# Optimization experiments

Measured on AMD Instinct MI355X. Metric: run time of the kernel, lower is better.

The kernel has to match this reference:

```python
import jax, jax.numpy as jnp
import numpy as np

N_NODES = 100000
N_EDGES = 1600000
IN_DIM, HID_DIM, OUT_DIM = 512, 128, 64


def gcn_layer(x, rows, cols, vals, W, b):
    # support = x @ W; out[i] = sum_{e: rows[e]==i} vals[e] * support[cols[e]] + b
    support = x @ W                      # [N, d_out]
    msgs = vals[:, None] * support[cols]  # [E, d_out] gather
    agg = jax.ops.segment_sum(msgs, rows, num_segments=N_NODES)  # scatter-add
    return agg + b


def setup_inputs() -> dict:
    key = jax.random.key(0)
    ks = jax.random.split(key, 8)
    x = jax.random.normal(ks[0], (N_NODES, IN_DIM), dtype=jnp.float32)
    edge_rows = jax.random.randint(ks[1], (N_EDGES,), 0, N_NODES, dtype=jnp.int32)
    edge_cols = jax.random.randint(ks[2], (N_EDGES,), 0, N_NODES, dtype=jnp.int32)
    edge_vals = jax.random.uniform(ks[3], (N_EDGES,), dtype=jnp.float32)
    W0 = jax.random.normal(ks[4], (IN_DIM, HID_DIM), dtype=jnp.float32) / np.sqrt(IN_DIM)
    b0 = jnp.zeros((HID_DIM,), dtype=jnp.float32)
    W1 = jax.random.normal(ks[5], (HID_DIM, OUT_DIM), dtype=jnp.float32) / np.sqrt(HID_DIM)
    b1 = jnp.zeros((OUT_DIM,), dtype=jnp.float32)
    return {"x": x, "edge_rows": edge_rows, "edge_cols": edge_cols,
            "edge_vals": edge_vals, "W0": W0, "b0": b0, "W1": W1, "b1": b1}


def reference(x, edge_rows, edge_cols, edge_vals, W0, b0, W1, b1):
    h = gcn_layer(x, edge_rows, edge_cols, edge_vals, W0, b0)  # GCN0
    h = jax.nn.relu(h)                                          # activation0
    # dropout: identity in eval mode
    out = gcn_layer(h, edge_rows, edge_cols, edge_vals, W1, b1)  # GCN1
    return out
```

## Files before the change

kernel.cpp:

```cpp
#include <hip/hip_runtime.h>

#define N_NODES 100000
#define N_EDGES 1600000
#define NBUCK   ((N_NODES + 127) / 128)
#define BCAP    4096

typedef __attribute__((ext_vector_type(8))) short bf16x8;
typedef __attribute__((ext_vector_type(4))) float f32x4;

__device__ __forceinline__ unsigned short f2bf(float f) {
    unsigned int u = __builtin_bit_cast(unsigned int, f);
    u = (u + 0x7FFFu + ((u >> 16) & 1u)) >> 16;
    return (unsigned short)u;
}
__device__ __forceinline__ float bfu2f(unsigned short u) {
    return __builtin_bit_cast(float, (unsigned int)u << 16);
}
__device__ __forceinline__ uint2 packbf4(float4 v) {
    uint2 p;
    p.x = (unsigned int)f2bf(v.x) | ((unsigned int)f2bf(v.y) << 16);
    p.y = (unsigned int)f2bf(v.z) | ((unsigned int)f2bf(v.w) << 16);
    return p;
}

__device__ __forceinline__ void block_barrier() {
    asm volatile("s_waitcnt lgkmcnt(0)" ::: "memory");
    __builtin_amdgcn_sched_barrier(0);
    __builtin_amdgcn_s_barrier();
    __builtin_amdgcn_sched_barrier(0);
}

__global__ __launch_bounds__(256) void prep_kernel(const float* __restrict__ W0,
                                                   const float* __restrict__ W1,
                                                   unsigned short* __restrict__ W0t,
                                                   unsigned short* __restrict__ W1t,
                                                   int* __restrict__ bcursor) {
    const int i = blockIdx.x * 256 + threadIdx.x;
    if (i < 512 * 128) {
        const int k = i / 128, c = i % 128;
        W0t[c * 512 + k] = f2bf(W0[i]);
    }
    const int j = i - 512 * 128;
    if (j >= 0 && j < 128 * 64) {
        const int k = j / 64, c = j % 64;
        W1t[c * 128 + k] = f2bf(W1[j]);
    }
    const int z = i - (512 * 128 + 128 * 64);
    if (z >= 0 && z < NBUCK) bcursor[z] = z * BCAP;
}

__global__ __launch_bounds__(256) void gemm1_kernel(const float* __restrict__ A,
                                                    const unsigned short* __restrict__ Wt,
                                                    unsigned short* __restrict__ C, int N) {
    constexpr int K   = 512;
    constexpr int M   = 128;
    constexpr int LDT = 40;

    __shared__ __align__(16) unsigned short As[2][64 * LDT];
    __shared__ __align__(16) unsigned short Bs[2][M * LDT];

    const int tid  = threadIdx.x;
    const int lane = tid & 63;
    const int wid  = tid >> 6;
    const int wm   = wid >> 1;
    const int wn   = wid & 1;
    const int brow = blockIdx.x * 64;

    const int ar0 = tid >> 3, akq = tid & 7;
    const int ar1 = ar0 + 32;
    const bool v0 = (brow + ar0) < N;
    const bool v1 = (brow + ar1) < N;
    const float* ap0 = A + (size_t)(brow + ar0) * K + akq * 4;
    const float* ap1 = A + (size_t)(brow + ar1) * K + akq * 4;
    const int br0 = tid >> 2, bkq = tid & 3;
    const unsigned short* bp0 = Wt + (size_t)br0 * K + bkq * 8;
    const unsigned short* bp1 = Wt + (size_t)(br0 + 64) * K + bkq * 8;

    float4 A0a, A0b, A1a, A1b, A2a, A2b, A3a, A3b;
    uint4  B0a, B0b, B1a, B1b, B2a, B2b, B3a, B3b;

#define ISSUE(s, t) do {                                                          \
        const int ko = (t) * 32;                                                  \
        A##s##a = v0 ? *reinterpret_cast<const float4*>(ap0 + ko)                 \
                     : make_float4(0.f, 0.f, 0.f, 0.f);                           \
        A##s##b = v1 ? *reinterpret_cast<const float4*>(ap1 + ko)                 \
                     : make_float4(0.f, 0.f, 0.f, 0.f);                           \
        B##s##a = *reinterpret_cast<const uint4*>(bp0 + ko);                      \
        B##s##b = *reinterpret_cast<const uint4*>(bp1 + ko);                      \
    } while (0)

#define WLDS(s, buf) do {                                                         \
        *reinterpret_cast<uint2*>(&As[buf][ar0 * LDT + akq * 4]) = packbf4(A##s##a); \
        *reinterpret_cast<uint2*>(&As[buf][ar1 * LDT + akq * 4]) = packbf4(A##s##b); \
        *reinterpret_cast<uint4*>(&Bs[buf][br0 * LDT + bkq * 8]) = B##s##a;          \
        *reinterpret_cast<uint4*>(&Bs[buf][(br0 + 64) * LDT + bkq * 8]) = B##s##b;   \
    } while (0)

    f32x4 acc[2][4];
#pragma unroll
    for (int m = 0; m < 2; ++m)
#pragma unroll
        for (int n = 0; n < 4; ++n) acc[m][n] = (f32x4){0.f, 0.f, 0.f, 0.f};

    const int afo = (wm * 32 + (lane & 15)) * LDT + (lane >> 4) * 8;
    const int bfo = (wn * 64 + (lane & 15)) * LDT + (lane >> 4) * 8;

    auto step = [&](int buf) {
        bf16x8 af[2], bfr[4];
#pragma unroll
        for (int m = 0; m < 2; ++m)
            af[m] = *reinterpret_cast<const bf16x8*>(&As[buf][afo + m * 16 * LDT]);
#pragma unroll
        for (int n = 0; n < 4; ++n)
            bfr[n] = *reinterpret_cast<const bf16x8*>(&Bs[buf][bfo + n * 16 * LDT]);
#pragma unroll
        for (int m = 0; m < 2; ++m)
#pragma unroll
            for (int n = 0; n < 4; ++n)
                acc[m][n] = __builtin_amdgcn_mfma_f32_16x16x32_bf16(af[m], bfr[n], acc[m][n], 0, 0, 0);
    };

    ISSUE(0, 0); ISSUE(1, 1); ISSUE(2, 2); ISSUE(3, 3);
    WLDS(0, 0);
    block_barrier();

#pragma unroll
    for (int i = 0; i < 4; ++i) {
        const int t = 4 * i;
        if (t + 4 < 16) ISSUE(0, t + 4);
        step(0);
        WLDS(1, 1);
        block_barrier();
        if (t + 5 < 16) ISSUE(1, t + 5);
        step(1);
        WLDS(2, 0);
        block_barrier();
        if (t + 6 < 16) ISSUE(2, t + 6);
        step(0);
        WLDS(3, 1);
        block_barrier();
        if (t + 7 < 16) ISSUE(3, t + 7);
        step(1);
        if (t + 4 < 16) WLDS(0, 0);
        block_barrier();
    }
#undef ISSUE
#undef WLDS

    const int rb = brow + wm * 32 + ((lane >> 4) * 4);
    const int cb = wn * 64 + (lane & 15);
#pragma unroll
    for (int m = 0; m < 2; ++m)
#pragma unroll
        for (int n = 0; n < 4; ++n)
#pragma unroll
            for (int j = 0; j < 4; ++j) {
                const int r = rb + m * 16 + j;
                if (r < N) C[(size_t)r * M + cb + n * 16] = f2bf(acc[m][n][j]);
            }
}

__global__ __launch_bounds__(256) void gemm2_kernel(const unsigned short* __restrict__ Hb,
                                                    const unsigned short* __restrict__ Wt,
                                                    unsigned short* __restrict__ C) {
    const int gw = (blockIdx.x * 256 + threadIdx.x) >> 6;
    if (gw >= N_NODES / 16) return;
    const int lane = threadIdx.x & 63;
    const int rlo = lane & 15, khi = lane >> 4;
    const int rb = gw * 16;

    const unsigned short* wp = Wt + (size_t)rlo * 128 + khi * 8;
    bf16x8 b[4][4];
#pragma unroll
    for (int n = 0; n < 4; ++n)
#pragma unroll
        for (int t = 0; t < 4; ++t)
            b[n][t] = *reinterpret_cast<const bf16x8*>(wp + (size_t)n * 16 * 128 + t * 32);

    f32x4 acc[4];
#pragma unroll
    for (int n = 0; n < 4; ++n) acc[n] = (f32x4){0.f, 0.f, 0.f, 0.f};

    const unsigned short* hp = Hb + (size_t)(rb + rlo) * 128 + khi * 8;
#pragma unroll
    for (int t = 0; t < 4; ++t) {
        const bf16x8 af = *reinterpret_cast<const bf16x8*>(hp + t * 32);
#pragma unroll
        for (int n = 0; n < 4; ++n)
            acc[n] = __builtin_amdgcn_mfma_f32_16x16x32_bf16(af, b[n][t], acc[n], 0, 0, 0);
    }

#pragma unroll
    for (int n = 0; n < 4; ++n)
#pragma unroll
        for (int j = 0; j < 4; ++j)
            C[(size_t)(rb + khi * 4 + j) * 64 + n * 16 + rlo] = f2bf(acc[n][j]);
}

#define SCAT_CH 4096
__global__ __launch_bounds__(256) void scatter_bucket_kernel(const int* __restrict__ rows,
                                                             const int* __restrict__ cols,
                                                             const float* __restrict__ vals,
                                                             int* __restrict__ bcursor,
                                                             int2* __restrict__ tmp) {
    __shared__ int hist[NBUCK];
    const int tid = threadIdx.x;
    const int e0  = blockIdx.x * SCAT_CH;

    int   er[16];
    int   ec[16];
    float ev[16];
#pragma unroll
    for (int i = 0; i < 16; ++i) {
        const int e = e0 + i * 256 + tid;
        const bool ok = e < N_EDGES;
        er[i] = ok ? rows[e] : -1;
        ec[i] = ok ? cols[e] : 0;
        ev[i] = ok ? vals[e] : 0.f;
    }

    for (int b = tid; b < NBUCK; b += 256) hist[b] = 0;
    __syncthreads();

#pragma unroll
    for (int i = 0; i < 16; ++i)
        if (er[i] >= 0) atomicAdd(&hist[er[i] >> 7], 1);
    __syncthreads();

    for (int b = tid; b < NBUCK; b += 256) {
        const int hcnt = hist[b];
        hist[b] = (hcnt > 0) ? atomicAdd(&bcursor[b], hcnt) : 0;
    }
    __syncthreads();

#pragma unroll
    for (int i = 0; i < 16; ++i) {
        if (er[i] >= 0) {
            const int pos = atomicAdd(&hist[er[i] >> 7], 1);
            tmp[pos] = make_int2(ec[i] | ((er[i] & 127) << 17), __float_as_int(ev[i]));
        }
    }
}

__global__ __launch_bounds__(256) void bucket_csr_kernel(const int* __restrict__ bcursor,
                                                         const int2* __restrict__ tmp,
                                                         int2* __restrict__ meta,
                                                         int2* __restrict__ row_range) {
    __shared__ int cnt_sh[128];
    __shared__ int startsh[128];
    __shared__ int cur[128];
    const int b   = blockIdx.x;
    const int tid = threadIdx.x;
    const int base = b * BCAP;
    const int cnt  = bcursor[b] - base;

    int2 w[16];
#pragma unroll
    for (int i = 0; i < 16; ++i) {
        const int j = i * 256 + tid;
        w[i] = (j < cnt) ? tmp[base + j] : make_int2(-1, 0);
    }

    if (tid < 128) cnt_sh[tid] = 0;
    __syncthreads();

#pragma unroll
    for (int i = 0; i < 16; ++i)
        if (w[i].x >= 0) atomicAdd(&cnt_sh[((unsigned int)w[i].x) >> 17], 1);
    __syncthreads();

    if (tid == 0) {
        int a = base;
        for (int i = 0; i < 128; ++i) { startsh[i] = a; a += cnt_sh[i]; }
    }
    __syncthreads();

    if (tid < 128) {
        cur[tid] = startsh[tid];
        const int row = (b << 7) + tid;
        if (row < N_NODES)
            row_range[row] = make_int2(startsh[tid], startsh[tid] + cnt_sh[tid]);
    }
    __syncthreads();

#pragma unroll
    for (int i = 0; i < 16; ++i) {
        if (w[i].x >= 0) {
            const int rl  = ((unsigned int)w[i].x) >> 17;
            const int pos = atomicAdd(&cur[rl], 1);
            meta[pos] = make_int2(w[i].x & 0x1FFFF, w[i].y);
        }
    }
}

template<int DIM, bool RELU_BF16_OUT>
__global__ __launch_bounds__(256) void spmm_kernel(const int2* __restrict__ row_range,
                                                   const int2* __restrict__ meta,
                                                   const unsigned short* __restrict__ sup,
                                                   const float* __restrict__ bias,
                                                   void* __restrict__ aggv) {
    const int wv = (blockIdx.x * 256 + threadIdx.x) >> 6;
    if (wv >= N_NODES) return;
    const int lane = threadIdx.x & 63;

    constexpr int GL = DIM / 8;
    constexpr int NG = 64 / GL;
    constexpr int UN = 2;
    const int grp = lane / GL;
    const int sub = lane % GL;

    const int2 rr = row_range[wv];
    const int start = rr.x, end = rr.y;

    float a[8] = {0.f, 0.f, 0.f, 0.f, 0.f, 0.f, 0.f, 0.f};

    int j = start + grp;
    while (j + (UN - 1) * NG < end) {
        int2 e[UN];
#pragma unroll
        for (int u = 0; u < UN; ++u) e[u] = meta[j + u * NG];
        bf16x8 s[UN];
#pragma unroll
        for (int u = 0; u < UN; ++u)
            s[u] = *reinterpret_cast<const bf16x8*>(sup + (size_t)e[u].x * DIM + sub * 8);
#pragma unroll
        for (int u = 0; u < UN; ++u) {
            const float v = __int_as_float(e[u].y);
#pragma unroll
            for (int d = 0; d < 8; ++d)
                a[d] = fmaf(v, bfu2f((unsigned short)s[u][d]), a[d]);
        }
        j += UN * NG;
    }
    for (; j < end; j += NG) {
        const int2 e = meta[j];
        const bf16x8 s = *reinterpret_cast<const bf16x8*>(sup + (size_t)e.x * DIM + sub * 8);
        const float v = __int_as_float(e.y);
#pragma unroll
        for (int d = 0; d < 8; ++d)
            a[d] = fmaf(v, bfu2f((unsigned short)s[d]), a[d]);
    }

#pragma unroll
    for (int d = 0; d < 8; ++d) {
        if (GL == 8) a[d] += __shfl_xor(a[d], 8);
        a[d] += __shfl_xor(a[d], 16);
        a[d] += __shfl_xor(a[d], 32);
    }

    if (lane < GL) {
        const float4 b0 = *reinterpret_cast<const float4*>(bias + sub * 8);
        const float4 b1 = *reinterpret_cast<const float4*>(bias + sub * 8 + 4);
        float o[8];
        o[0] = a[0] + b0.x; o[1] = a[1] + b0.y; o[2] = a[2] + b0.z; o[3] = a[3] + b0.w;
        o[4] = a[4] + b1.x; o[5] = a[5] + b1.y; o[6] = a[6] + b1.z; o[7] = a[7] + b1.w;
        if (RELU_BF16_OUT) {
            unsigned short* h = (unsigned short*)aggv;
            bf16x8 r;
#pragma unroll
            for (int d = 0; d < 8; ++d) r[d] = (short)f2bf(fmaxf(o[d], 0.f));
            *reinterpret_cast<bf16x8*>(h + (size_t)wv * DIM + sub * 8) = r;
        } else {
            float* og = (float*)aggv;
            float* dst = og + (size_t)wv * DIM + sub * 8;
            *reinterpret_cast<float4*>(dst)     = make_float4(o[0], o[1], o[2], o[3]);
            *reinterpret_cast<float4*>(dst + 4) = make_float4(o[4], o[5], o[6], o[7]);
        }
    }
}

extern "C" void kernel_launch(void* const* d_in, const int* in_sizes, int n_in,
                              void* d_out, int out_size, void* d_ws, size_t ws_size,
                              hipStream_t stream) {
    const float* x    = (const float*)d_in[0];
    const int*   rows = (const int*)d_in[1];
    const int*   cols = (const int*)d_in[2];
    const float* vals = (const float*)d_in[3];
    const float* W0   = (const float*)d_in[4];
    const float* b0   = (const float*)d_in[5];
    const float* W1   = (const float*)d_in[6];
    const float* b1   = (const float*)d_in[7];
    float*       out  = (float*)d_out;

    char* p = (char*)d_ws;
    unsigned short* sup0 = (unsigned short*)p;  p += (size_t)N_NODES * 128 * 2;
    unsigned short* h    = (unsigned short*)p;  p += (size_t)N_NODES * 128 * 2;
    unsigned short* sup1 = (unsigned short*)p;  p += (size_t)N_NODES * 64 * 2;
    unsigned short* W0t  = (unsigned short*)p;  p += (size_t)512 * 128 * 2;
    unsigned short* W1t  = (unsigned short*)p;  p += (size_t)128 * 64 * 2;
    int*   bcursor  = (int*)p;                  p += (size_t)((NBUCK + 3) / 4) * 16;
    int2*  row_range= (int2*)p;                 p += (size_t)N_NODES * 8;
    int2*  tmp      = (int2*)p;                 p += (size_t)NBUCK * BCAP * 8;
    int2*  meta     = (int2*)p;                 p += (size_t)NBUCK * BCAP * 8;

    const int prep_blocks = (512 * 128 + 128 * 64 + NBUCK + 255) / 256;
    const int scat_blocks = (N_EDGES + SCAT_CH - 1) / SCAT_CH;
    const int gemm_blocks = (N_NODES + 63) / 64;
    const int gem2_blocks = (N_NODES / 16 + 3) / 4;
    const int spmm_blocks = (N_NODES * 64 + 255) / 256;

    prep_kernel<<<prep_blocks, 256, 0, stream>>>(W0, W1, W0t, W1t, bcursor);

    scatter_bucket_kernel<<<scat_blocks, 256, 0, stream>>>(rows, cols, vals, bcursor, tmp);
    bucket_csr_kernel<<<NBUCK, 256, 0, stream>>>(bcursor, tmp, meta, row_range);

    gemm1_kernel<<<gemm_blocks, 256, 0, stream>>>(x, W0t, sup0, N_NODES);
    spmm_kernel<128, true><<<spmm_blocks, 256, 0, stream>>>(row_range, meta, sup0, b0, h);

    gemm2_kernel<<<gem2_blocks, 256, 0, stream>>>(h, W1t, sup1);
    spmm_kernel<64, false><<<spmm_blocks, 256, 0, stream>>>(row_range, meta, sup1, b1, out);
}
```

Baseline: 224.4 us.

## Fuse per-bucket CSR construction into SpMM using shared-memory edge sort

```diff
diff --git a/kernel.cpp b/kernel.cpp
--- a/kernel.cpp
+++ b/kernel.cpp
@@ -242,129 +242,116 @@
     }
 }
 
-__global__ __launch_bounds__(256) void bucket_csr_kernel(const int* __restrict__ bcursor,
-                                                         const int2* __restrict__ tmp,
-                                                         int2* __restrict__ meta,
-                                                         int2* __restrict__ row_range) {
-    __shared__ int cnt_sh[128];
-    __shared__ int startsh[128];
-    __shared__ int cur[128];
-    const int b   = blockIdx.x;
-    const int tid = threadIdx.x;
+template<int DIM, bool RELU_BF16_OUT>
+__global__ __launch_bounds__(512) void spmm_bucket_kernel(const int* __restrict__ bcursor,
+                                                          const int2* __restrict__ tmp,
+                                                          const unsigned short* __restrict__ sup,
+                                                          const float* __restrict__ bias,
+                                                          void* __restrict__ aggv) {
+    constexpr int GL = DIM / 8;
+    constexpr int NG = 64 / GL;
+
+    __shared__ int2 eds[BCAP];
+    __shared__ int  cnt_sh[128];
+    __shared__ int  startsh[128];
+    __shared__ int  cur[128];
+
+    const int b    = blockIdx.x;
+    const int tid  = threadIdx.x;
     const int base = b * BCAP;
     const int cnt  = bcursor[b] - base;
 
-    int2 w[16];
-#pragma unroll
-    for (int i = 0; i < 16; ++i) {
-        const int j = i * 256 + tid;
+    int2 w[8];
+#pragma unroll
+    for (int i = 0; i < 8; ++i) {
+        const int j = i * 512 + tid;
         w[i] = (j < cnt) ? tmp[base + j] : make_int2(-1, 0);
     }
-
     if (tid < 128) cnt_sh[tid] = 0;
     __syncthreads();
-
-#pragma unroll
-    for (int i = 0; i < 16; ++i)
+#pragma unroll
+    for (int i = 0; i < 8; ++i)
         if (w[i].x >= 0) atomicAdd(&cnt_sh[((unsigned int)w[i].x) >> 17], 1);
     __syncthreads();
 
     if (tid == 0) {
-        int a = base;
+        int a = 0;
         for (int i = 0; i < 128; ++i) { startsh[i] = a; a += cnt_sh[i]; }
     }
     __syncthreads();
-
-    if (tid < 128) {
-        cur[tid] = startsh[tid];
-        const int row = (b << 7) + tid;
-        if (row < N_NODES)
-            row_range[row] = make_int2(startsh[tid], startsh[tid] + cnt_sh[tid]);
-    }
-    __syncthreads();
-
-#pragma unroll
-    for (int i = 0; i < 16; ++i) {
+    if (tid < 128) cur[tid] = startsh[tid];
+    __syncthreads();
+
+#pragma unroll
+    for (int i = 0; i < 8; ++i) {
         if (w[i].x >= 0) {
             const int rl  = ((unsigned int)w[i].x) >> 17;
             const int pos = atomicAdd(&cur[rl], 1);
-            meta[pos] = make_int2(w[i].x & 0x1FFFF, w[i].y);
-        }
-    }
-}
-
-template<int DIM, bool RELU_BF16_OUT>
-__global__ __launch_bounds__(256) void spmm_kernel(const int2* __restrict__ row_range,
-                                                   const int2* __restrict__ meta,
-                                                   const unsigned short* __restrict__ sup,
-                                                   const float* __restrict__ bias,
-                                                   void* __restrict__ aggv) {
-    const int wv = (blockIdx.x * 256 + threadIdx.x) >> 6;
-    if (wv >= N_NODES) return;
-    const int lane = threadIdx.x & 63;
-
-    constexpr int GL = DIM / 8;
-    constexpr int NG = 64 / GL;
-    constexpr int UN = 2;
-    const int grp = lane / GL;
-    const int sub = lane % GL;
-
-    const int2 rr = row_range[wv];
-    const int start = rr.x, end = rr.y;
-
-    float a[8] = {0.f, 0.f, 0.f, 0.f, 0.f, 0.f, 0.f, 0.f};
-
-    int j = start + grp;
-    while (j + (UN - 1) * NG < end) {
-        int2 e[UN];
-#pragma unroll
-        for (int u = 0; u < UN; ++u) e[u] = meta[j + u * NG];
-        bf16x8 s[UN];
-#pragma unroll
-        for (int u = 0; u < UN; ++u)
-            s[u] = *reinterpret_cast<const bf16x8*>(sup + (size_t)e[u].x * DIM + sub * 8);
-#pragma unroll
-        for (int u = 0; u < UN; ++u) {
-            const float v = __int_as_float(e[u].y);
-#pragma unroll
-            for (int d = 0; d < 8; ++d)
-                a[d] = fmaf(v, bfu2f((unsigned short)s[u][d]), a[d]);
-        }
-        j += UN * NG;
-    }
-    for (; j < end; j += NG) {
-        const int2 e = meta[j];
-        const bf16x8 s = *reinterpret_cast<const bf16x8*>(sup + (size_t)e.x * DIM + sub * 8);
-        const float v = __int_as_float(e.y);
-#pragma unroll
-        for (int d = 0; d < 8; ++d)
-            a[d] = fmaf(v, bfu2f((unsigned short)s[d]), a[d]);
-    }
-
-#pragma unroll
-    for (int d = 0; d < 8; ++d) {
-        if (GL == 8) a[d] += __shfl_xor(a[d], 8);
-        a[d] += __shfl_xor(a[d], 16);
-        a[d] += __shfl_xor(a[d], 32);
-    }
-
-    if (lane < GL) {
-        const float4 b0 = *reinterpret_cast<const float4*>(bias + sub * 8);
-        const float4 b1 = *reinterpret_cast<const float4*>(bias + sub * 8 + 4);
-        float o[8];
-        o[0] = a[0] + b0.x; o[1] = a[1] + b0.y; o[2] = a[2] + b0.z; o[3] = a[3] + b0.w;
-        o[4] = a[4] + b1.x; o[5] = a[5] + b1.y; o[6] = a[6] + b1.z; o[7] = a[7] + b1.w;
-        if (RELU_BF16_OUT) {
-            unsigned short* h = (unsigned short*)aggv;
-            bf16x8 r;
-#pragma unroll
-            for (int d = 0; d < 8; ++d) r[d] = (short)f2bf(fmaxf(o[d], 0.f));
-            *reinterpret_cast<bf16x8*>(h + (size_t)wv * DIM + sub * 8) = r;
-        } else {
-            float* og = (float*)aggv;
-            float* dst = og + (size_t)wv * DIM + sub * 8;
-            *reinterpret_cast<float4*>(dst)     = make_float4(o[0], o[1], o[2], o[3]);
-            *reinterpret_cast<float4*>(dst + 4) = make_float4(o[4], o[5], o[6], o[7]);
+            eds[pos] = make_int2(w[i].x & 0x1FFFF, w[i].y);
+        }
+    }
+    __syncthreads();
+
+    const int lane = tid & 63;
+    const int wid  = tid >> 6;
+    const int grp  = lane / GL;
+    const int sub  = lane % GL;
+
+    for (int r8 = 0; r8 < 16; ++r8) {
+        const int rl  = wid * 16 + r8;
+        const int row = (b << 7) + rl;
+        const int start = startsh[rl];
+        const int end   = start + cnt_sh[rl];
+
+        float a[8] = {0.f, 0.f, 0.f, 0.f, 0.f, 0.f, 0.f, 0.f};
+
+        int j = start + grp;
+        while (j + NG < end) {
+            const int2 e0 = eds[j];
+            const int2 e1 = eds[j + NG];
+            const bf16x8 s0 = *reinterpret_cast<const bf16x8*>(sup + (size_t)e0.x * DIM + sub * 8);
+            const bf16x8 s1 = *reinterpret_cast<const bf16x8*>(sup + (size_t)e1.x * DIM + sub * 8);
+            const float v0 = __int_as_float(e0.y);
+            const float v1 = __int_as_float(e1.y);
+#pragma unroll
+            for (int d = 0; d < 8; ++d) a[d] = fmaf(v0, bfu2f((unsigned short)s0[d]), a[d]);
+#pragma unroll
+            for (int d = 0; d < 8; ++d) a[d] = fmaf(v1, bfu2f((unsigned short)s1[d]), a[d]);
+            j += 2 * NG;
+        }
+        for (; j < end; j += NG) {
+            const int2 e = eds[j];
+            const bf16x8 s = *reinterpret_cast<const bf16x8*>(sup + (size_t)e.x * DIM + sub * 8);
+            const float v = __int_as_float(e.y);
+#pragma unroll
+            for (int d = 0; d < 8; ++d) a[d] = fmaf(v, bfu2f((unsigned short)s[d]), a[d]);
+        }
+
+#pragma unroll
+        for (int d = 0; d < 8; ++d) {
+            if (GL == 8) a[d] += __shfl_xor(a[d], 8);
+            a[d] += __shfl_xor(a[d], 16);
+            a[d] += __shfl_xor(a[d], 32);
+        }
+
+        if (lane < GL && row < N_NODES) {
+            const float4 b0 = *reinterpret_cast<const float4*>(bias + sub * 8);
+            const float4 b1 = *reinterpret_cast<const float4*>(bias + sub * 8 + 4);
+            float o[8];
+            o[0] = a[0] + b0.x; o[1] = a[1] + b0.y; o[2] = a[2] + b0.z; o[3] = a[3] + b0.w;
+            o[4] = a[4] + b1.x; o[5] = a[5] + b1.y; o[6] = a[6] + b1.z; o[7] = a[7] + b1.w;
+            if (RELU_BF16_OUT) {
+                unsigned short* hb = (unsigned short*)aggv;
+                bf16x8 r;
+#pragma unroll
+                for (int d = 0; d < 8; ++d) r[d] = (short)f2bf(fmaxf(o[d], 0.f));
+                *reinterpret_cast<bf16x8*>(hb + (size_t)row * DIM + sub * 8) = r;
+            } else {
+                float* og = (float*)aggv;
+                float* dst = og + (size_t)row * DIM + sub * 8;
+                *reinterpret_cast<float4*>(dst)     = make_float4(o[0], o[1], o[2], o[3]);
+                *reinterpret_cast<float4*>(dst + 4) = make_float4(o[4], o[5], o[6], o[7]);
+            }
         }
     }
 }
@@ -389,24 +376,20 @@
     unsigned short* W0t  = (unsigned short*)p;  p += (size_t)512 * 128 * 2;
     unsigned short* W1t  = (unsigned short*)p;  p += (size_t)128 * 64 * 2;
     int*   bcursor  = (int*)p;                  p += (size_t)((NBUCK + 3) / 4) * 16;
-    int2*  row_range= (int2*)p;                 p += (size_t)N_NODES * 8;
     int2*  tmp      = (int2*)p;                 p += (size_t)NBUCK * BCAP * 8;
-    int2*  meta     = (int2*)p;                 p += (size_t)NBUCK * BCAP * 8;
 
     const int prep_blocks = (512 * 128 + 128 * 64 + NBUCK + 255) / 256;
     const int scat_blocks = (N_EDGES + SCAT_CH - 1) / SCAT_CH;
     const int gemm_blocks = (N_NODES + 63) / 64;
     const int gem2_blocks = (N_NODES / 16 + 3) / 4;
-    const int spmm_blocks = (N_NODES * 64 + 255) / 256;
 
     prep_kernel<<<prep_blocks, 256, 0, stream>>>(W0, W1, W0t, W1t, bcursor);
 
     scatter_bucket_kernel<<<scat_blocks, 256, 0, stream>>>(rows, cols, vals, bcursor, tmp);
-    bucket_csr_kernel<<<NBUCK, 256, 0, stream>>>(bcursor, tmp, meta, row_range);
 
     gemm1_kernel<<<gemm_blocks, 256, 0, stream>>>(x, W0t, sup0, N_NODES);
-    spmm_kernel<128, true><<<spmm_blocks, 256, 0, stream>>>(row_range, meta, sup0, b0, h);
+    spmm_bucket_kernel<128, true><<<NBUCK, 512, 0, stream>>>(bcursor, tmp, sup0, b0, h);
 
     gemm2_kernel<<<gem2_blocks, 256, 0, stream>>>(h, W1t, sup1);
-    spmm_kernel<64, false><<<spmm_blocks, 256, 0, stream>>>(row_range, meta, sup1, b1, out);
-}
+    spmm_bucket_kernel<64, false><<<NBUCK, 512, 0, stream>>>(bcursor, tmp, sup1, b1, out);
+}
```

Result: faster. 218.7 us (-2.5%).
